# Performance work log

Measured on AMD Instinct MI355X. Metric: run time of the kernel, lower is better.

The kernel has to match this reference:

```python
import jax, jax.numpy as jnp
import numpy as np

PS = 5    # patch_w for rgb arch
K = 14    # num nearest neighbors
WS = 29   # search window side


def _patchify(img_pad, H, W):
    """img_pad: [t, H+2*(whalf+phalf), W+..., c] channels-last.
    Returns patch features over the search grid: [t, H+2*whalf, W+2*whalf, PS*PS*c]."""
    whalf = WS // 2
    Hg, Wg = H + 2 * whalf, W + 2 * whalf
    slices = [img_pad[:, dy:dy + Hg, dx:dx + Wg, :]
              for dy in range(PS) for dx in range(PS)]
    return jnp.concatenate(slices, axis=-1)


def _forward(noisy, sigma):
    t, c, H, W = noisy.shape
    # rescale to [-1,1] and remove per-frame channel means (as in forward)
    x = (noisy / 255.0 - 0.5) / 0.5
    means = x.mean((-2, -1), keepdims=True)
    x = x - means
    xl = jnp.transpose(x, (0, 2, 3, 1))  # [t,H,W,c]

    phalf, whalf = PS // 2, WS // 2
    pad = phalf + whalf
    xp = jnp.pad(xl, ((0, 0), (pad, pad), (pad, pad), (0, 0)), mode='reflect')

    P = _patchify(xp, H, W)              # [t, H+2*whalf, W+2*whalf, D]
    D = PS * PS * c
    Pq = P[:, whalf:whalf + H, whalf:whalf + W, :]  # query patches [t,H,W,D]

    # --- windowed kNN patch search: scan over WS*WS offsets ---
    def dist_step(_, o):
        oy, ox = o // WS, o % WS
        Pn = jax.lax.dynamic_slice(P, (0, oy, ox, 0), (t, H, W, D))
        d = jnp.sum((Pq - Pn) ** 2, axis=-1)  # [t,H,W]
        return None, d

    _, dists = jax.lax.scan(dist_step, None, jnp.arange(WS * WS))
    dists = jnp.transpose(dists, (1, 2, 3, 0))  # [t,H,W,WS*WS]

    negv, idx = jax.lax.top_k(-dists, K)        # k smallest distances
    dk = -negv                                   # [t,H,W,K]
    oy, ox = idx // WS, idx % WS

    # --- gather neighbor patches ---
    rows = jnp.arange(H)[None, :, None, None] + oy   # [t,H,W,K]
    cols = jnp.arange(W)[None, None, :, None] + ox
    ti = jnp.arange(t)[:, None, None, None]
    neigh = P[ti, rows, cols]                        # [t,H,W,K,D]

    # --- patch denoise: distance-softmax weighted neighbor aggregation ---
    sig = (jnp.float32(sigma) / 255.0) / 0.5
    beta = 1.0 / (2.0 * sig * sig * D)
    wts = jax.nn.softmax(-beta * dk, axis=-1)        # [t,H,W,K]
    pdeno = jnp.einsum('thwk,thwkd->thwd', wts, neigh)  # [t,H,W,D]
    patches = pdeno.reshape(t, H, W, PS, PS, c)

    # --- weighted iFold: overlap-add + count normalization ---
    acc = jnp.zeros((t, H + 2 * phalf, W + 2 * phalf, c), x.dtype)
    cnt = jnp.zeros((t, H + 2 * phalf, W + 2 * phalf, 1), x.dtype)
    ones = jnp.ones((t, H, W, 1), x.dtype)
    for py in range(PS):
        for px in range(PS):
            acc = acc.at[:, py:py + H, px:px + W, :].add(patches[:, :, :, py, px, :])
            cnt = cnt.at[:, py:py + H, px:px + W, :].add(ones)
    deno = acc / cnt
    deno = deno[:, phalf:H + phalf, phalf:W + phalf, :]  # final_format crop

    deno = jnp.transpose(deno, (0, 3, 1, 2)) + means
    deno = 255.0 * (deno * 0.5 + 0.5)
    return deno


def setup_inputs() -> dict:
    key = jax.random.key(0)
    k1, _ = jax.random.split(key)
    noisy = jax.random.uniform(k1, (4, 3, 128, 128), dtype=jnp.float32) * 255.0
    sigma = 25
    return {"noisy": noisy, "sigma": sigma}


def reference(noisy, sigma):
    return _forward(noisy, sigma)
```

## Files before the change

### kernel.cpp

```cpp
#include <hip/hip_runtime.h>

#define T_ 4
#define H_ 128
#define W_ 128
#define XPS 160
#define WSZ 29
#define K_ 14
#define ACCS 132

#define SROWS 4
#define SCOLS 12
#define TR 36
#define TC 44
#define RS 136
#define NBI 32
#define NBJ 11
#define NW 4
#define OPW 211

#define HS 40
#define N2S 48

#define DPP_SHL(x, n) __uint_as_float((unsigned)__builtin_amdgcn_update_dpp( \
        0, (int)__float_as_uint(x), 0x100 + (n), 0xF, 0xF, true))

__global__ void k_means(const float* __restrict__ noisy, float* __restrict__ means) {
    int tc = blockIdx.x;
    const float* src = noisy + (size_t)tc * (H_ * W_);
    float s = 0.f;
    for (int i = threadIdx.x; i < H_ * W_; i += 256) s += src[i];
    __shared__ float red[256];
    red[threadIdx.x] = s;
    __syncthreads();
    for (int st = 128; st > 0; st >>= 1) {
        if ((int)threadIdx.x < st) red[threadIdx.x] += red[threadIdx.x + st];
        __syncthreads();
    }
    if (threadIdx.x == 0)
        means[tc] = red[0] * (1.f / (H_ * W_)) * (2.f / 255.f) - 1.f;
}

__global__ void k_pad(const float* __restrict__ noisy, const float* __restrict__ means,
                      float* __restrict__ xp) {
    int idx = blockIdx.x * 256 + threadIdx.x;
    if (idx >= T_ * XPS * XPS) return;
    int t  = idx / (XPS * XPS);
    int rr = (idx / XPS) % XPS;
    int cc = idx % XPS;
    int ry = rr - 16; if (ry < 0) ry = -ry; if (ry > H_ - 1) ry = 2 * (H_ - 1) - ry;
    int rx = cc - 16; if (rx < 0) rx = -rx; if (rx > W_ - 1) rx = 2 * (W_ - 1) - rx;
    float* dst = xp + (size_t)idx * 3;
#pragma unroll
    for (int c = 0; c < 3; c++) {
        float v = noisy[(((size_t)t * 3 + c) * H_ + ry) * W_ + rx];
        dst[c] = v * (2.f / 255.f) - 1.f - means[t * 3 + c];
    }
}

__global__ __launch_bounds__(256, 4)
void k_main(const float* __restrict__ xp, const int* __restrict__ sigma_p,
            float* __restrict__ acc) {
    __shared__ __align__(16) float tileF[TR * RS];
    __shared__ unsigned kbuf[NW * K_][49];
    __shared__ float N2s[32 * N2S];

    const int tid = threadIdx.x;
    const int b   = blockIdx.x;
    const int t   = b / (NBI * NBJ);
    const int rem = b % (NBI * NBJ);
    const int bi  = (rem / NBJ) * SROWS;
    const int bj  = (rem % NBJ) * SCOLS;

    const float* src = xp + ((size_t)(t * XPS + bi) * XPS + bj) * 3;
    for (int i = tid; i < TR * 33; i += 256) {
        int rr = i / 33, q = i - rr * 33;
        float4 v = *reinterpret_cast<const float4*>(src + (size_t)rr * (XPS * 3) + q * 4);
        *reinterpret_cast<float4*>(&tileF[rr * RS + q * 4]) = v;
    }
    __syncthreads();

    float* hbuf = reinterpret_cast<float*>(&kbuf[0][0]);
    for (int i = tid; i < TR * HS; i += 256) {
        int r = i / HS, c = i - (i / HS) * HS;
        const float* tp = &tileF[r * RS + c * 3];
        float s = 0.f;
#pragma unroll
        for (int d = 0; d < 15; d++) { float v = tp[d]; s = fmaf(v, v, s); }
        hbuf[i] = s;
    }
    __syncthreads();

    for (int i = tid; i < 32 * HS; i += 256) {
        int r = i / HS, c = i - (i / HS) * HS;
        const float* hp = &hbuf[r * HS + c];
        N2s[r * N2S + c] = hp[0] + hp[HS] + hp[2 * HS] + hp[3 * HS] + hp[4 * HS];
    }
    __syncthreads();

    const int w    = tid >> 6;
    const int lane = tid & 63;
    const int g    = lane >> 4;
    const int tj   = lane & 15;
    const bool valid = (tj < SCOLS) && (bj + tj < W_);

    float A[5][3];
#pragma unroll
    for (int dy = 0; dy < 5; dy++)
#pragma unroll
        for (int c = 0; c < 3; c++)
            A[dy][c] = tileF[(14 + g + dy) * RS + (14 + tj) * 3 + c];
    const float N2q = N2s[(g + 14) * N2S + (tj + 14)];

    unsigned keys[K_];
#pragma unroll
    for (int k = 0; k < K_; k++) keys[k] = 0xFFFFFF00u + k;
    unsigned kmax = 0xFFFFFF00u + (K_ - 1);

    const int o0 = w * OPW;
    const int on = (o0 + OPW <= WSZ * WSZ) ? OPW : (WSZ * WSZ - o0);
    for (int i = 0; i < on; i++) {
        int o  = o0 + i;
        int oy = o / WSZ;
        int ox = o - oy * WSZ;
        const float* bp = &tileF[(g + oy) * RS + (tj + ox) * 3];
        float cb = 0.f;
#pragma unroll
        for (int dy = 0; dy < 5; dy++) {
            cb = fmaf(A[dy][0], bp[dy * RS + 0], cb);
            cb = fmaf(A[dy][1], bp[dy * RS + 1], cb);
            cb = fmaf(A[dy][2], bp[dy * RS + 2], cb);
        }
        float CB = cb;
        CB += DPP_SHL(cb, 1);
        CB += DPP_SHL(cb, 2);
        CB += DPP_SHL(cb, 3);
        CB += DPP_SHL(cb, 4);
        float D = fmaf(-2.f, CB, N2q + N2s[(g + oy) * N2S + (tj + ox)]);
        D = fmaxf(D, 0.f);
        unsigned key = (__float_as_uint(D) & 0xFFFFFC00u) | (unsigned)o;
        if (valid && key < kmax) {
#pragma unroll
            for (int k = 0; k < K_; k++) keys[k] = (keys[k] == kmax) ? key : keys[k];
            kmax = keys[0];
#pragma unroll
            for (int k = 1; k < K_; k++) kmax = keys[k] > kmax ? keys[k] : kmax;
        }
    }

    __syncthreads();
    const int pxi = g * SCOLS + tj;
    if (valid) {
#pragma unroll
        for (int k = 0; k < K_; k++) kbuf[w * K_ + k][pxi] = keys[k];
    }
#pragma unroll
    for (int k = 0; k < K_; k++) keys[k] = 0xFFFFFF00u + k;
    kmax = 0xFFFFFF00u + (K_ - 1);
    __syncthreads();

    if (valid) {
        for (int j = 0; j < NW * K_; j++) {
            unsigned key = kbuf[j][pxi];
            if (key < kmax) {
#pragma unroll
                for (int k = 0; k < K_; k++) keys[k] = (keys[k] == kmax) ? key : keys[k];
                kmax = keys[0];
#pragma unroll
                for (int k = 1; k < K_; k++) kmax = keys[k] > kmax ? keys[k] : kmax;
            }
        }
    }

    float sig  = (float)sigma_p[0] * (2.f / 255.f);
    float beta = 1.f / (2.f * sig * sig * 75.f);
    float wk[K_];
    int oyk[K_], oxk[K_];
    float dmin = 3.4e38f;
#pragma unroll
    for (int k = 0; k < K_; k++) {
        float dv = __uint_as_float(keys[k] & 0xFFFFFC00u);
        wk[k] = dv;
        int ok = (int)(keys[k] & 1023u);
        oyk[k] = ok / WSZ;
        oxk[k] = ok - oyk[k] * WSZ;
        dmin = fminf(dmin, dv);
    }
    float sw = 0.f;
#pragma unroll
    for (int k = 0; k < K_; k++) { float e = __expf(beta * (dmin - wk[k])); wk[k] = e; sw += e; }
    float inv = 1.f / sw;
#pragma unroll
    for (int k = 0; k < K_; k++) wk[k] *= inv;

    __syncthreads();
    float* accb = reinterpret_cast<float*>(&kbuf[0][0]);
    for (int i = tid; i < 8 * 16 * 3; i += 256) accb[i] = 0.f;
    __syncthreads();

    for (int p = w; p < 25; p += NW) {
        int py = p / 5, px = p - py * 5;
        if (valid) {
            float s0 = 0.f, s1 = 0.f, s2 = 0.f;
#pragma unroll
            for (int k = 0; k < K_; k++) {
                const float* nb = &tileF[(g + oyk[k] + py) * RS + (tj + oxk[k] + px) * 3];
                s0 += wk[k] * nb[0];
                s1 += wk[k] * nb[1];
                s2 += wk[k] * nb[2];
            }
            float* ap = accb + ((g + py) * 16 + (tj + px)) * 3;
            atomicAdd(ap + 0, s0);
            atomicAdd(ap + 1, s1);
            atomicAdd(ap + 2, s2);
        }
    }
    __syncthreads();

    for (int i = tid; i < 8 * 16 * 3; i += 256) {
        int ch = i % 3;
        int cc = (i / 3) & 15;
        int rr = i / 48;
        int gr = bi + rr, gc = bj + cc;
        if (gc < ACCS)
            atomicAdd(&acc[(((size_t)t * ACCS + gr) * ACCS + gc) * 3 + ch], accb[i]);
    }
}

__global__ void k_final(const float* __restrict__ acc, const float* __restrict__ means,
                        float* __restrict__ out) {
    int idx = blockIdx.x * 256 + threadIdx.x;
    if (idx >= T_ * 3 * H_ * W_) return;
    int j  = idx & 127;
    int i  = (idx >> 7) & 127;
    int ch = (idx >> 14) % 3;
    int t  = idx / (3 * H_ * W_);
    int r = i + 2, s = j + 2;
    int ny = (r < 4 ? r : 4) - (r > 127 ? r - 127 : 0) + 1;
    int nx = (s < 4 ? s : 4) - (s > 127 ? s - 127 : 0) + 1;
    float v = acc[(((size_t)t * ACCS + r) * ACCS + s) * 3 + ch] / (float)(ny * nx);
    v += means[t * 3 + ch];
    out[idx] = 127.5f * v + 127.5f;
}

extern "C" void kernel_launch(void* const* d_in, const int* in_sizes, int n_in,
                              void* d_out, int out_size, void* d_ws, size_t ws_size,
                              hipStream_t stream) {
    (void)in_sizes; (void)n_in; (void)out_size; (void)ws_size;
    const float* noisy = (const float*)d_in[0];
    const int*   sigma = (const int*)d_in[1];

    float* means = (float*)d_ws;
    float* xp    = means + 64;
    float* acc   = xp + (size_t)T_ * XPS * XPS * 3;
    float* out   = (float*)d_out;

    hipLaunchKernelGGL(k_means, dim3(12), dim3(256), 0, stream, noisy, means);
    hipLaunchKernelGGL(k_pad, dim3((T_ * XPS * XPS + 255) / 256), dim3(256), 0, stream,
                       noisy, means, xp);
    hipMemsetAsync(acc, 0, (size_t)T_ * ACCS * ACCS * 3 * sizeof(float), stream);
    hipLaunchKernelGGL(k_main, dim3(T_ * NBI * NBJ), dim3(256), 0, stream, xp, sigma, acc);
    hipLaunchKernelGGL(k_final, dim3((T_ * 3 * H_ * W_ + 255) / 256), dim3(256), 0, stream,
                       acc, means, out);
}
```

Before: 305.0 us.

## Use branchless sorted-insert top-k and row-split offset loop

Replaces the conditional replace-max top-k update with a branchless sorted insertion network (min/max chain) that runs on every candidate, removing the divergent branch and max recomputation. The offset loop is restructured into nested oy/ox loops with the work split by whole rows across the four waves, removing per-offset division and using incremental pointers. The FMA reduction is split into three independent accumulators and the DPP reduction is shortened. N2S stride is narrowed to 40. In exchange, the insertion now does about 27 min/max operations on every candidate, including invalid lanes, rather than only on candidates that beat the current max.

```diff
diff --git a/kernel.cpp b/kernel.cpp
--- a/kernel.cpp
+++ b/kernel.cpp
@@ -11,7 +11,6 @@
 #define SROWS 4
 #define SCOLS 12
 #define TR 36
-#define TC 44
 #define RS 136
 #define NBI 32
 #define NBJ 11
@@ -19,10 +18,18 @@
 #define OPW 211
 
 #define HS 40
-#define N2S 48
+#define N2S 40
 
 #define DPP_SHL(x, n) __uint_as_float((unsigned)__builtin_amdgcn_update_dpp( \
         0, (int)__float_as_uint(x), 0x100 + (n), 0xF, 0xF, true))
+
+#define SORTED_INSERT(s, key)                                        \
+    do {                                                             \
+        _Pragma("unroll")                                            \
+        for (int _i = K_ - 1; _i >= 1; _i--)                         \
+            s[_i] = min(max(key, s[_i - 1]), s[_i]);                 \
+        s[0] = min(s[0], key);                                       \
+    } while (0)
 
 __global__ void k_means(const float* __restrict__ noisy, float* __restrict__ means) {
     int tc = blockIdx.x;
@@ -111,39 +118,32 @@
             A[dy][c] = tileF[(14 + g + dy) * RS + (14 + tj) * 3 + c];
     const float N2q = N2s[(g + 14) * N2S + (tj + 14)];
 
-    unsigned keys[K_];
-#pragma unroll
-    for (int k = 0; k < K_; k++) keys[k] = 0xFFFFFF00u + k;
-    unsigned kmax = 0xFFFFFF00u + (K_ - 1);
-
-    const int o0 = w * OPW;
-    const int on = (o0 + OPW <= WSZ * WSZ) ? OPW : (WSZ * WSZ - o0);
-    for (int i = 0; i < on; i++) {
-        int o  = o0 + i;
-        int oy = o / WSZ;
-        int ox = o - oy * WSZ;
-        const float* bp = &tileF[(g + oy) * RS + (tj + ox) * 3];
-        float cb = 0.f;
-#pragma unroll
-        for (int dy = 0; dy < 5; dy++) {
-            cb = fmaf(A[dy][0], bp[dy * RS + 0], cb);
-            cb = fmaf(A[dy][1], bp[dy * RS + 1], cb);
-            cb = fmaf(A[dy][2], bp[dy * RS + 2], cb);
-        }
-        float CB = cb;
-        CB += DPP_SHL(cb, 1);
-        CB += DPP_SHL(cb, 2);
-        CB += DPP_SHL(cb, 3);
-        CB += DPP_SHL(cb, 4);
-        float D = fmaf(-2.f, CB, N2q + N2s[(g + oy) * N2S + (tj + ox)]);
-        D = fmaxf(D, 0.f);
-        unsigned key = (__float_as_uint(D) & 0xFFFFFC00u) | (unsigned)o;
-        if (valid && key < kmax) {
-#pragma unroll
-            for (int k = 0; k < K_; k++) keys[k] = (keys[k] == kmax) ? key : keys[k];
-            kmax = keys[0];
-#pragma unroll
-            for (int k = 1; k < K_; k++) kmax = keys[k] > kmax ? keys[k] : kmax;
+    unsigned s[K_];
+#pragma unroll
+    for (int k = 0; k < K_; k++) s[k] = 0xFFFFFF00u + k;
+
+    const int oy0 = (w == 0) ? 0 : 8 + 7 * (w - 1);
+    const int oy1 = (w == 0) ? 8 : 8 + 7 * w;
+    for (int oy = oy0; oy < oy1; oy++) {
+        const float* bp = &tileF[(g + oy) * RS + tj * 3];
+        const float* np = &N2s[(g + oy) * N2S + tj];
+        int o = oy * WSZ;
+        for (int ox = 0; ox < WSZ; ox++, o++, bp += 3, np++) {
+            float c0 = 0.f, c1 = 0.f, c2 = 0.f;
+#pragma unroll
+            for (int dy = 0; dy < 5; dy++) {
+                c0 = fmaf(A[dy][0], bp[dy * RS + 0], c0);
+                c1 = fmaf(A[dy][1], bp[dy * RS + 1], c1);
+                c2 = fmaf(A[dy][2], bp[dy * RS + 2], c2);
+            }
+            float cb = (c0 + c1) + c2;
+            float a2 = cb + DPP_SHL(cb, 1);
+            float a4 = a2 + DPP_SHL(a2, 2);
+            float CB = a4 + DPP_SHL(cb, 4);
+            float D = fmaf(-2.f, CB, N2q + np[0]);
+            D = fmaxf(D, 0.f);
+            unsigned key = (__float_as_uint(D) & 0xFFFFFC00u) | (unsigned)o;
+            SORTED_INSERT(s, key);
         }
     }
 
@@ -151,23 +151,16 @@
     const int pxi = g * SCOLS + tj;
     if (valid) {
 #pragma unroll
-        for (int k = 0; k < K_; k++) kbuf[w * K_ + k][pxi] = keys[k];
-    }
-#pragma unroll
-    for (int k = 0; k < K_; k++) keys[k] = 0xFFFFFF00u + k;
-    kmax = 0xFFFFFF00u + (K_ - 1);
+        for (int k = 0; k < K_; k++) kbuf[w * K_ + k][pxi] = s[k];
+    }
+#pragma unroll
+    for (int k = 0; k < K_; k++) s[k] = 0xFFFFFF00u + k;
     __syncthreads();
 
     if (valid) {
         for (int j = 0; j < NW * K_; j++) {
             unsigned key = kbuf[j][pxi];
-            if (key < kmax) {
-#pragma unroll
-                for (int k = 0; k < K_; k++) keys[k] = (keys[k] == kmax) ? key : keys[k];
-                kmax = keys[0];
-#pragma unroll
-                for (int k = 1; k < K_; k++) kmax = keys[k] > kmax ? keys[k] : kmax;
-            }
+            SORTED_INSERT(s, key);
         }
     }
 
@@ -175,15 +168,13 @@
     float beta = 1.f / (2.f * sig * sig * 75.f);
     float wk[K_];
     int oyk[K_], oxk[K_];
-    float dmin = 3.4e38f;
+    const float dmin = __uint_as_float(s[0] & 0xFFFFFC00u);
 #pragma unroll
     for (int k = 0; k < K_; k++) {
-        float dv = __uint_as_float(keys[k] & 0xFFFFFC00u);
-        wk[k] = dv;
-        int ok = (int)(keys[k] & 1023u);
+        wk[k] = __uint_as_float(s[k] & 0xFFFFFC00u);
+        int ok = (int)(s[k] & 1023u);
         oyk[k] = ok / WSZ;
         oxk[k] = ok - oyk[k] * WSZ;
-        dmin = fminf(dmin, dv);
     }
     float sw = 0.f;
 #pragma unroll
```

Measured after the change: 299.1 us. No clear change (-1.9%).
